# Kernel tuning notes

Measured on AMD Instinct MI355X. Metric: run time of the kernel, lower is better.

The kernel has to match this reference:

```python
import jax, jax.numpy as jnp
import numpy as np

N_DEV, N_CAT, N_APP = 100, 1000, 100000
D = 256
E = 100000

EDGES = [("dev", "app", "ei_dev_app", "ew_dev_app"),
         ("app", "cat", "ei_app_cat", "ew_app_cat"),
         ("app", "app", "ei_app_app", "ew_app_app")]
SIZES = {"dev": N_DEV, "cat": N_CAT, "app": N_APP}


def setup_inputs() -> dict:
    key = jax.random.key(0)
    ks = jax.random.split(key, 32)
    s = 1.0 / np.sqrt(D)
    inp = {
        "x_dev": jax.random.normal(ks[0], (N_DEV, D), jnp.float32),
        "x_cat": jax.random.normal(ks[1], (N_CAT, D), jnp.float32),
        "x_app": jax.random.normal(ks[2], (N_APP, D), jnp.float32),
        "ei_dev_app": jnp.stack([jax.random.randint(ks[3], (E,), 0, N_DEV),
                                 jax.random.randint(ks[4], (E,), 0, N_APP)]).astype(jnp.int32),
        "ei_app_cat": jnp.stack([jax.random.randint(ks[5], (E,), 0, N_APP),
                                 jax.random.randint(ks[6], (E,), 0, N_CAT)]).astype(jnp.int32),
        "ei_app_app": jnp.stack([jax.random.randint(ks[7], (E,), 0, N_APP),
                                 jax.random.randint(ks[8], (E,), 0, N_APP)]).astype(jnp.int32),
        "ew_dev_app": jax.random.uniform(ks[9], (E,), jnp.float32, 0.5, 2.0),
        "ew_app_cat": jax.random.uniform(ks[10], (E,), jnp.float32, 0.5, 2.0),
        "ew_app_app": jax.random.uniform(ks[11], (E,), jnp.float32, 0.5, 2.0),
    }
    # per-node-type linear params for layer1 and layer2 (torch nn.Linear equivalents)
    i = 12
    for layer in (1, 2):
        for t in ("dev", "cat", "app"):
            inp[f"W{layer}_{t}"] = jax.random.normal(ks[i], (D, D), jnp.float32) * s
            inp[f"b{layer}_{t}"] = jax.random.normal(ks[i + 1], (D,), jnp.float32) * s
            i += 2
    return inp


def _mp_layer(x, params, ei, ew):
    """One MyMessagePassing layer: per-src-type linear+relu, edge-weighted
    gather, scatter-add into destination node type."""
    # src-type transform (same math as doing it per edge-type iteration)
    h = {t: jax.nn.relu(x[t] @ params[t][0] + params[t][1]) for t in x}
    out = {t: jnp.zeros((SIZES[t], D), x[t].dtype) for t in x}
    for src, dst, ei_name, ew_name in EDGES:
        idx = ei[ei_name]
        msg = h[src][idx[0]] * ew[ew_name][:, None]  # [E, D]
        out[dst] = out[dst] + jax.ops.segment_sum(msg, idx[1], num_segments=SIZES[dst])
    return out


def reference(x_dev, x_cat, x_app,
              ei_dev_app, ei_app_cat, ei_app_app,
              ew_dev_app, ew_app_cat, ew_app_app,
              W1_dev, b1_dev, W1_cat, b1_cat, W1_app, b1_app,
              W2_dev, b2_dev, W2_cat, b2_cat, W2_app, b2_app):
    ei = {"ei_dev_app": ei_dev_app, "ei_app_cat": ei_app_cat, "ei_app_app": ei_app_app}
    ew = {"ew_dev_app": ew_dev_app, "ew_app_cat": ew_app_cat, "ew_app_app": ew_app_app}
    x = {"dev": x_dev, "cat": x_cat, "app": x_app}
    p1 = {"dev": (W1_dev, b1_dev), "cat": (W1_cat, b1_cat), "app": (W1_app, b1_app)}
    p2 = {"dev": (W2_dev, b2_dev), "cat": (W2_cat, b2_cat), "app": (W2_app, b2_app)}
    x = _mp_layer(x, p1, ei, ew)
    x = _mp_layer(x, p2, ei, ew)
    return (x["dev"], x["cat"], x["app"])
```

## Files before the change

kernel.cpp:

```cpp
#include <hip/hip_runtime.h>
#include <cstdint>
#include <cstddef>

#define DD 256
constexpr int NDEV = 100;
constexpr int NCAT = 1000;
constexpr int NAPP = 100000;
constexpr int NE   = 100000;
constexpr int NCNT = NAPP + NAPP + NCAT;

typedef __attribute__((ext_vector_type(8))) short  bf16x8;
typedef __attribute__((ext_vector_type(8))) unsigned short ushort8;
typedef __attribute__((ext_vector_type(4))) float  f32x4;

__device__ __forceinline__ unsigned short f2bf(float f) {
    unsigned int u = __float_as_uint(f);
    u += 0x7fffu + ((u >> 16) & 1u);
    return (unsigned short)(u >> 16);
}
__device__ __forceinline__ float bf2f(unsigned short h) {
    return __uint_as_float((unsigned int)h << 16);
}

__global__ __launch_bounds__(256)
void wsplit_kernel(const float* __restrict__ W, unsigned short* __restrict__ hi,
                   unsigned short* __restrict__ lo) {
    const int idx = blockIdx.x * 256 + threadIdx.x;
    const int k = idx >> 8, n = idx & 255;
    const float f = W[idx];
    const unsigned short h = f2bf(f);
    hi[n * 256 + k] = h;
    lo[n * 256 + k] = f2bf(f - bf2f(h));
}

#define BK 32
#define PAD 40

__global__ __launch_bounds__(256, 2)
void linear_relu_mfma_kernel(const float* __restrict__ A,
                             const unsigned short* __restrict__ Wt_hi,
                             const unsigned short* __restrict__ Wt_lo,
                             const float* __restrict__ bias,
                             float* __restrict__ C, int M) {
    __shared__ unsigned short As_hi[128][PAD];
    __shared__ unsigned short As_lo[128][PAD];
    __shared__ unsigned short Ws_hi[256][PAD];
    __shared__ unsigned short Ws_lo[256][PAD];

    const int t    = threadIdx.x;
    const int wave = t >> 6;
    const int lane = t & 63;
    const int cl   = lane & 15;
    const int kg8  = (lane >> 4) * 8;
    const int m0   = blockIdx.x * 128;
    const int n0w  = wave * 64;

    f32x4 acc[8][4];
#pragma unroll
    for (int m = 0; m < 8; ++m)
#pragma unroll
        for (int n = 0; n < 4; ++n) acc[m][n] = (f32x4){0.f, 0.f, 0.f, 0.f};

    const int ar = t >> 1;
    const int ak = (t & 1) * 16;

    for (int k0 = 0; k0 < DD; k0 += BK) {
        {
            float fv[16];
            if (m0 + ar < M) {
                const float* p = A + (size_t)(m0 + ar) * DD + k0 + ak;
#pragma unroll
                for (int i = 0; i < 4; ++i) {
                    const float4 v = *(const float4*)(p + i * 4);
                    fv[i * 4 + 0] = v.x; fv[i * 4 + 1] = v.y;
                    fv[i * 4 + 2] = v.z; fv[i * 4 + 3] = v.w;
                }
            } else {
#pragma unroll
                for (int i = 0; i < 16; ++i) fv[i] = 0.f;
            }
#pragma unroll
            for (int g = 0; g < 2; ++g) {
                ushort8 hh, ll;
#pragma unroll
                for (int j = 0; j < 8; ++j) {
                    const float f = fv[g * 8 + j];
                    const unsigned short h = f2bf(f);
                    hh[j] = h;
                    ll[j] = f2bf(f - bf2f(h));
                }
                *(ushort8*)&As_hi[ar][ak + g * 8] = hh;
                *(ushort8*)&As_lo[ar][ak + g * 8] = ll;
            }
        }
        {
            const unsigned short* ph = Wt_hi + (size_t)t * DD + k0;
            const unsigned short* pl = Wt_lo + (size_t)t * DD + k0;
#pragma unroll
            for (int g = 0; g < 4; ++g) {
                *(ushort8*)&Ws_hi[t][g * 8] = *(const ushort8*)(ph + g * 8);
                *(ushort8*)&Ws_lo[t][g * 8] = *(const ushort8*)(pl + g * 8);
            }
        }
        __syncthreads();

        bf16x8 ah[8], al[8], bb[4];
#pragma unroll
        for (int m = 0; m < 8; ++m) {
            ah[m] = *(const bf16x8*)&As_hi[m * 16 + cl][kg8];
            al[m] = *(const bf16x8*)&As_lo[m * 16 + cl][kg8];
        }
#pragma unroll
        for (int n = 0; n < 4; ++n)
            bb[n] = *(const bf16x8*)&Ws_hi[n0w + n * 16 + cl][kg8];
#pragma unroll
        for (int m = 0; m < 8; ++m)
#pragma unroll
            for (int n = 0; n < 4; ++n)
                acc[m][n] = __builtin_amdgcn_mfma_f32_16x16x32_bf16(
                    ah[m], bb[n], acc[m][n], 0, 0, 0);
#pragma unroll
        for (int m = 0; m < 8; ++m)
#pragma unroll
            for (int n = 0; n < 4; ++n)
                acc[m][n] = __builtin_amdgcn_mfma_f32_16x16x32_bf16(
                    al[m], bb[n], acc[m][n], 0, 0, 0);
#pragma unroll
        for (int n = 0; n < 4; ++n)
            bb[n] = *(const bf16x8*)&Ws_lo[n0w + n * 16 + cl][kg8];
#pragma unroll
        for (int m = 0; m < 8; ++m)
#pragma unroll
            for (int n = 0; n < 4; ++n)
                acc[m][n] = __builtin_amdgcn_mfma_f32_16x16x32_bf16(
                    ah[m], bb[n], acc[m][n], 0, 0, 0);
        __syncthreads();
    }

    const int r4 = (lane >> 4) << 2;
#pragma unroll
    for (int n = 0; n < 4; ++n) {
        const int col = n0w + n * 16 + cl;
        const float bv = bias[col];
#pragma unroll
        for (int m = 0; m < 8; ++m) {
            const int rowb = m0 + m * 16 + r4;
            float* cp = C + (size_t)rowb * DD + col;
#pragma unroll
            for (int j = 0; j < 4; ++j)
                if (rowb + j < M) cp[(size_t)j * DD] = fmaxf(acc[m][n][j] + bv, 0.f);
        }
    }
}

__global__ __launch_bounds__(256)
void linear_relu_kernel(const float* __restrict__ A, const float* __restrict__ W,
                        const float* __restrict__ bias, float* __restrict__ C,
                        int M) {
    __shared__ float As[8][128];
    __shared__ float Bs[8][128];

    const int t  = threadIdx.x;
    const int m0 = blockIdx.x * 128;
    const int n0 = blockIdx.y * 128;
    const int ra = (t >> 4) << 2;
    const int ca = (t & 15) << 2;

    float acc[8][8];
#pragma unroll
    for (int i = 0; i < 8; ++i)
#pragma unroll
        for (int j = 0; j < 8; ++j) acc[i][j] = 0.f;

    for (int k0 = 0; k0 < DD; k0 += 8) {
        {
            const int row = t >> 1;
            const int kk  = (t & 1) << 2;
            float4 v = make_float4(0.f, 0.f, 0.f, 0.f);
            if (m0 + row < M)
                v = *(const float4*)(A + (size_t)(m0 + row) * DD + k0 + kk);
            As[kk + 0][row] = v.x;
            As[kk + 1][row] = v.y;
            As[kk + 2][row] = v.z;
            As[kk + 3][row] = v.w;
        }
        {
            const int kk = t >> 5;
            const int nn = (t & 31) << 2;
            *(float4*)&Bs[kk][nn] =
                *(const float4*)(W + (size_t)(k0 + kk) * DD + n0 + nn);
        }
        __syncthreads();
#pragma unroll
        for (int k = 0; k < 8; ++k) {
            const float4 a0 = *(const float4*)&As[k][ra];
            const float4 a1 = *(const float4*)&As[k][ra + 64];
            const float4 b0 = *(const float4*)&Bs[k][ca];
            const float4 b1 = *(const float4*)&Bs[k][ca + 64];
            const float av[8] = {a0.x, a0.y, a0.z, a0.w, a1.x, a1.y, a1.z, a1.w};
            const float bv[8] = {b0.x, b0.y, b0.z, b0.w, b1.x, b1.y, b1.z, b1.w};
#pragma unroll
            for (int i = 0; i < 8; ++i)
#pragma unroll
                for (int j = 0; j < 8; ++j)
                    acc[i][j] = fmaf(av[i], bv[j], acc[i][j]);
        }
        __syncthreads();
    }

    const float4 bias0 = *(const float4*)(bias + n0 + ca);
    const float4 bias1 = *(const float4*)(bias + n0 + ca + 64);
#pragma unroll
    for (int i = 0; i < 8; ++i) {
        const int row = m0 + ((i < 4) ? (ra + i) : (ra + 64 + i - 4));
        if (row >= M) continue;
        float4 o0, o1;
        o0.x = fmaxf(acc[i][0] + bias0.x, 0.f);
        o0.y = fmaxf(acc[i][1] + bias0.y, 0.f);
        o0.z = fmaxf(acc[i][2] + bias0.z, 0.f);
        o0.w = fmaxf(acc[i][3] + bias0.w, 0.f);
        o1.x = fmaxf(acc[i][4] + bias1.x, 0.f);
        o1.y = fmaxf(acc[i][5] + bias1.y, 0.f);
        o1.z = fmaxf(acc[i][6] + bias1.z, 0.f);
        o1.w = fmaxf(acc[i][7] + bias1.w, 0.f);
        *(float4*)(C + (size_t)row * DD + n0 + ca)      = o0;
        *(float4*)(C + (size_t)row * DD + n0 + ca + 64) = o1;
    }
}

__global__ __launch_bounds__(256)
void hist3_kernel(const int* __restrict__ d_aa, const int* __restrict__ d_da,
                  const int* __restrict__ d_ac, int* __restrict__ counts) {
    const int g = blockIdx.x * 256 + threadIdx.x;
    if (g < NE)            atomicAdd(&counts[d_aa[g]], 1);
    else if (g < 2 * NE)   atomicAdd(&counts[NAPP + d_da[g - NE]], 1);
    else if (g < 3 * NE)   atomicAdd(&counts[2 * NAPP + d_ac[g - 2 * NE]], 1);
}

__global__ __launch_bounds__(256)
void scan_partial_kernel(const int* __restrict__ counts, int* __restrict__ bsum,
                         int n) {
    __shared__ int sd[256];
    const int t   = threadIdx.x;
    const int idx = blockIdx.x * 1024 + t * 4;
    int s = 0;
    if (idx + 3 < n) {
        const int4 c = *(const int4*)(counts + idx);
        s = c.x + c.y + c.z + c.w;
    } else {
        for (int j = 0; j < 4; ++j) if (idx + j < n) s += counts[idx + j];
    }
    sd[t] = s;
    __syncthreads();
    for (int off = 128; off > 0; off >>= 1) {
        if (t < off) sd[t] += sd[t + off];
        __syncthreads();
    }
    if (t == 0) bsum[blockIdx.x] = sd[0];
}

__global__ __launch_bounds__(256)
void scan_bsum_kernel(const int* __restrict__ bsum, int* __restrict__ boff, int nb) {
    __shared__ int sd[256];
    const int t = threadIdx.x;
    const int v = (t < nb) ? bsum[t] : 0;
    sd[t] = v;
    __syncthreads();
    for (int off = 1; off < 256; off <<= 1) {
        const int w = (t >= off) ? sd[t - off] : 0;
        __syncthreads();
        sd[t] += w;
        __syncthreads();
    }
    if (t < nb) boff[t] = sd[t] - v;
}

__global__ __launch_bounds__(256)
void scan_apply_kernel(int* __restrict__ counts, const int* __restrict__ boff,
                       int* __restrict__ rs, int n) {
    __shared__ int sd[256];
    const int t   = threadIdx.x;
    const int idx = blockIdx.x * 1024 + t * 4;
    int c[4] = {0, 0, 0, 0};
    if (idx + 3 < n) {
        const int4 v = *(const int4*)(counts + idx);
        c[0] = v.x; c[1] = v.y; c[2] = v.z; c[3] = v.w;
    } else {
        for (int j = 0; j < 4; ++j) if (idx + j < n) c[j] = counts[idx + j];
    }
    const int s = c[0] + c[1] + c[2] + c[3];
    sd[t] = s;
    __syncthreads();
    for (int off = 1; off < 256; off <<= 1) {
        const int w = (t >= off) ? sd[t - off] : 0;
        __syncthreads();
        sd[t] += w;
        __syncthreads();
    }
    int o = boff[blockIdx.x] + sd[t] - s;
#pragma unroll
    for (int j = 0; j < 4; ++j) {
        const int i = idx + j;
        if (i < n) {
            rs[i]     = o;
            counts[i] = o;
            o += c[j];
            if (i == n - 1) rs[n] = o;
        }
    }
}

__global__ __launch_bounds__(256)
void fill3_kernel(const int* __restrict__ ei_aa, const float* __restrict__ ew_aa,
                  const int* __restrict__ ei_da, const float* __restrict__ ew_da,
                  const int* __restrict__ ei_ac, const float* __restrict__ ew_ac,
                  int* __restrict__ cursor, int* __restrict__ srcs,
                  float* __restrict__ wsorted) {
    const int g = blockIdx.x * 256 + threadIdx.x;
    if (g >= 3 * NE) return;
    const int*   ei;
    const float* ew;
    int e, base;
    if (g < NE)            { ei = ei_aa; ew = ew_aa; e = g;          base = 0; }
    else if (g < 2 * NE)   { ei = ei_da; ew = ew_da; e = g - NE;     base = NAPP; }
    else                   { ei = ei_ac; ew = ew_ac; e = g - 2 * NE; base = 2 * NAPP; }
    const int d   = ei[NE + e];
    const int pos = atomicAdd(&cursor[base + d], 1);
    srcs[pos]    = ei[e];
    wsorted[pos] = ew[e];
}

__global__ __launch_bounds__(256)
void gather_l1_app_kernel(const float* __restrict__ hA, const float* __restrict__ hD,
                          const int* __restrict__ rsA, const int* __restrict__ rsD,
                          const int* __restrict__ s, const float* __restrict__ w,
                          float* __restrict__ out, int ndst) {
    const int d    = (int)((blockIdx.x * 256 + threadIdx.x) >> 6);
    const int lane = threadIdx.x & 63;
    if (d >= ndst) return;
    const int o = lane << 2;
    float4 acc = make_float4(0.f, 0.f, 0.f, 0.f);
    for (int p = rsA[d], pe = rsA[d + 1]; p < pe; ++p) {
        const float  ww = w[p];
        const float4 v  = *(const float4*)(hA + (size_t)s[p] * DD + o);
        acc.x = fmaf(ww, v.x, acc.x);
        acc.y = fmaf(ww, v.y, acc.y);
        acc.z = fmaf(ww, v.z, acc.z);
        acc.w = fmaf(ww, v.w, acc.w);
    }
    for (int p = rsD[d], pe = rsD[d + 1]; p < pe; ++p) {
        const float  ww = w[p];
        const float4 v  = *(const float4*)(hD + (size_t)s[p] * DD + o);
        acc.x = fmaf(ww, v.x, acc.x);
        acc.y = fmaf(ww, v.y, acc.y);
        acc.z = fmaf(ww, v.z, acc.z);
        acc.w = fmaf(ww, v.w, acc.w);
    }
    *(float4*)(out + (size_t)d * DD + o) = acc;
}

__global__ __launch_bounds__(256)
void gather_l2_app_kernel(const float* __restrict__ hA,
                          const int* __restrict__ rsA, const int* __restrict__ rsD,
                          const int* __restrict__ s, const float* __restrict__ w,
                          const float* __restrict__ b2dev,
                          float* __restrict__ out, int ndst) {
    const int d    = (int)((blockIdx.x * 256 + threadIdx.x) >> 6);
    const int lane = threadIdx.x & 63;
    if (d >= ndst) return;
    const int o = lane << 2;
    float4 acc = make_float4(0.f, 0.f, 0.f, 0.f);
    for (int p = rsA[d], pe = rsA[d + 1]; p < pe; ++p) {
        const float  ww = w[p];
        const float4 v  = *(const float4*)(hA + (size_t)s[p] * DD + o);
        acc.x = fmaf(ww, v.x, acc.x);
        acc.y = fmaf(ww, v.y, acc.y);
        acc.z = fmaf(ww, v.z, acc.z);
        acc.w = fmaf(ww, v.w, acc.w);
    }
    float wsum = 0.f;
    for (int p = rsD[d], pe = rsD[d + 1]; p < pe; ++p) wsum += w[p];
    const float4 b = *(const float4*)(b2dev + o);
    acc.x = fmaf(wsum, fmaxf(b.x, 0.f), acc.x);
    acc.y = fmaf(wsum, fmaxf(b.y, 0.f), acc.y);
    acc.z = fmaf(wsum, fmaxf(b.z, 0.f), acc.z);
    acc.w = fmaf(wsum, fmaxf(b.w, 0.f), acc.w);
    *(float4*)(out + (size_t)d * DD + o) = acc;
}

__global__ __launch_bounds__(256)
void gather_cat_kernel(const float* __restrict__ hA,
                       const int* __restrict__ rs, const int* __restrict__ s,
                       const float* __restrict__ w,
                       float* __restrict__ out, int ndst) {
    const int d    = (int)((blockIdx.x * 256 + threadIdx.x) >> 6);
    const int lane = threadIdx.x & 63;
    if (d >= ndst) return;
    const int o = lane << 2;
    float4 acc = make_float4(0.f, 0.f, 0.f, 0.f);
    for (int p = rs[d], pe = rs[d + 1]; p < pe; ++p) {
        const float  ww = w[p];
        const float4 v  = *(const float4*)(hA + (size_t)s[p] * DD + o);
        acc.x = fmaf(ww, v.x, acc.x);
        acc.y = fmaf(ww, v.y, acc.y);
        acc.z = fmaf(ww, v.z, acc.z);
        acc.w = fmaf(ww, v.w, acc.w);
    }
    *(float4*)(out + (size_t)d * DD + o) = acc;
}

extern "C" void kernel_launch(void* const* d_in, const int* in_sizes, int n_in,
                              void* d_out, int out_size, void* d_ws, size_t ws_size,
                              hipStream_t stream) {
    const float* x_dev  = (const float*)d_in[0];
    const float* x_app  = (const float*)d_in[2];
    const int*   ei_da  = (const int*)d_in[3];
    const int*   ei_ac  = (const int*)d_in[4];
    const int*   ei_aa  = (const int*)d_in[5];
    const float* ew_da  = (const float*)d_in[6];
    const float* ew_ac  = (const float*)d_in[7];
    const float* ew_aa  = (const float*)d_in[8];
    const float* W1_dev = (const float*)d_in[9];
    const float* b1_dev = (const float*)d_in[10];
    const float* W1_app = (const float*)d_in[13];
    const float* b1_app = (const float*)d_in[14];
    const float* b2_dev = (const float*)d_in[16];
    const float* W2_app = (const float*)d_in[19];
    const float* b2_app = (const float*)d_in[20];

    float* out     = (float*)d_out;
    float* out_cat = out + (size_t)NDEV * DD;
    float* out_app = out + (size_t)(NDEV + NCAT) * DD;

    float* h_app  = (float*)d_ws;
    float* h_dev  = h_app + (size_t)NAPP * DD;
    int*   counts = (int*)(h_dev + (size_t)NDEV * DD);
    int*   rs_all = counts + NCNT;
    int*   s_all  = rs_all + NCNT + 1;
    float* w_all  = (float*)(s_all + 3 * NE);
    int*   bsum   = (int*)(w_all + 3 * NE);
    int*   boff   = bsum + 256;

    int* rs_aa = rs_all;
    int* rs_da = rs_all + NAPP;
    int* rs_ac = rs_all + 2 * NAPP;

    unsigned short* wt1_hi = (unsigned short*)counts;
    unsigned short* wt1_lo = wt1_hi + 65536;
    unsigned short* wt2_hi = wt1_lo + 65536;
    unsigned short* wt2_lo = wt2_hi + 65536;

    const int  nblk = (NCNT + 1023) / 1024;
    const int  gMfma = (NAPP + 127) / 128;
    const int  gGatherApp = (NAPP + 3) / 4;
    const int  gGatherCat = (NCAT + 3) / 4;
    const int  g3e = (3 * NE + 255) / 256;

    hipMemsetAsync(counts, 0, (size_t)NCNT * sizeof(int), stream);
    hist3_kernel<<<g3e, 256, 0, stream>>>(ei_aa + NE, ei_da + NE, ei_ac + NE, counts);
    scan_partial_kernel<<<nblk, 256, 0, stream>>>(counts, bsum, NCNT);
    scan_bsum_kernel<<<1, 256, 0, stream>>>(bsum, boff, nblk);
    scan_apply_kernel<<<nblk, 256, 0, stream>>>(counts, boff, rs_all, NCNT);
    fill3_kernel<<<g3e, 256, 0, stream>>>(ei_aa, ew_aa, ei_da, ew_da, ei_ac, ew_ac,
                                          counts, s_all, w_all);

    wsplit_kernel<<<256, 256, 0, stream>>>(W1_app, wt1_hi, wt1_lo);
    wsplit_kernel<<<256, 256, 0, stream>>>(W2_app, wt2_hi, wt2_lo);

    linear_relu_mfma_kernel<<<gMfma, 256, 0, stream>>>(x_app, wt1_hi, wt1_lo,
                                                       b1_app, h_app, NAPP);
    linear_relu_kernel<<<dim3(1, 2), 256, 0, stream>>>(x_dev, W1_dev, b1_dev,
                                                       h_dev, NDEV);
    gather_l1_app_kernel<<<gGatherApp, 256, 0, stream>>>(
        h_app, h_dev, rs_aa, rs_da, s_all, w_all, out_app, NAPP);

    linear_relu_mfma_kernel<<<gMfma, 256, 0, stream>>>(out_app, wt2_hi, wt2_lo,
                                                       b2_app, h_app, NAPP);
    gather_l2_app_kernel<<<gGatherApp, 256, 0, stream>>>(
        h_app, rs_aa, rs_da, s_all, w_all, b2_dev, out_app, NAPP);
    gather_cat_kernel<<<gGatherCat, 256, 0, stream>>>(
        h_app, rs_ac, s_all, w_all, out_cat, NCAT);

    hipMemsetAsync(out, 0, (size_t)NDEV * DD * sizeof(float), stream);
}
```

Measured before the change: 641.2 us.

## Retile split-bf16 MFMA GEMM to 128x128 blocks with register-prefetched A tiles

The linear+relu MFMA kernel now uses a 2D grid with 128x128 output tiles and a 2x2 wave layout, each wave computing 64x64. Weight fragments are read straight from global memory (L2-resident) instead of being staged in LDS, and the A tile for the next k-step is prefetched into registers while MFMAs run. LDS shrinks to the A hi/lo tiles in an MFMA-friendly layout, so occupancy can rise to 3 blocks per CU. The cost is that A is converted twice (once per column block) and more global weight loads are issued.

```diff
diff --git a/kernel.cpp b/kernel.cpp
--- a/kernel.cpp
+++ b/kernel.cpp
@@ -33,118 +33,129 @@
     lo[n * 256 + k] = f2bf(f - bf2f(h));
 }
 
-#define BK 32
-#define PAD 40
-
-__global__ __launch_bounds__(256, 2)
+__global__ __launch_bounds__(256, 3)
 void linear_relu_mfma_kernel(const float* __restrict__ A,
                              const unsigned short* __restrict__ Wt_hi,
                              const unsigned short* __restrict__ Wt_lo,
                              const float* __restrict__ bias,
                              float* __restrict__ C, int M) {
-    __shared__ unsigned short As_hi[128][PAD];
-    __shared__ unsigned short As_lo[128][PAD];
-    __shared__ unsigned short Ws_hi[256][PAD];
-    __shared__ unsigned short Ws_lo[256][PAD];
+    __shared__ unsigned short As_hi[4096];
+    __shared__ unsigned short As_lo[4096];
 
     const int t    = threadIdx.x;
-    const int wave = t >> 6;
+    const int wid  = t >> 6;
     const int lane = t & 63;
+    const int wr   = wid >> 1;
+    const int wc   = wid & 1;
     const int cl   = lane & 15;
-    const int kg8  = (lane >> 4) * 8;
+    const int kg   = lane >> 4;
     const int m0   = blockIdx.x * 128;
-    const int n0w  = wave * 64;
-
-    f32x4 acc[8][4];
-#pragma unroll
-    for (int m = 0; m < 8; ++m)
+    const int nb   = blockIdx.y * 128 + wc * 64;
+
+    const int loff = kg * 128 + cl * 8;
+
+    const int sr = t >> 1;
+    const int sk = (t & 1) * 16;
+    const bool arow_ok = (m0 + sr) < M;
+    const float* ap = A + (size_t)(m0 + sr) * DD + sk;
+    const int wbase = (sr >> 4) * 512 + (sr & 15) * 8;
+    const int kgw   = (sk >> 3);
+
+    f32x4 acc[4][4];
+#pragma unroll
+    for (int m = 0; m < 4; ++m)
 #pragma unroll
         for (int n = 0; n < 4; ++n) acc[m][n] = (f32x4){0.f, 0.f, 0.f, 0.f};
 
-    const int ar = t >> 1;
-    const int ak = (t & 1) * 16;
-
-    for (int k0 = 0; k0 < DD; k0 += BK) {
-        {
-            float fv[16];
-            if (m0 + ar < M) {
-                const float* p = A + (size_t)(m0 + ar) * DD + k0 + ak;
-#pragma unroll
-                for (int i = 0; i < 4; ++i) {
-                    const float4 v = *(const float4*)(p + i * 4);
-                    fv[i * 4 + 0] = v.x; fv[i * 4 + 1] = v.y;
-                    fv[i * 4 + 2] = v.z; fv[i * 4 + 3] = v.w;
-                }
-            } else {
-#pragma unroll
-                for (int i = 0; i < 16; ++i) fv[i] = 0.f;
-            }
-#pragma unroll
-            for (int g = 0; g < 2; ++g) {
-                ushort8 hh, ll;
-#pragma unroll
-                for (int j = 0; j < 8; ++j) {
-                    const float f = fv[g * 8 + j];
-                    const unsigned short h = f2bf(f);
-                    hh[j] = h;
-                    ll[j] = f2bf(f - bf2f(h));
-                }
-                *(ushort8*)&As_hi[ar][ak + g * 8] = hh;
-                *(ushort8*)&As_lo[ar][ak + g * 8] = ll;
-            }
-        }
-        {
-            const unsigned short* ph = Wt_hi + (size_t)t * DD + k0;
-            const unsigned short* pl = Wt_lo + (size_t)t * DD + k0;
-#pragma unroll
-            for (int g = 0; g < 4; ++g) {
-                *(ushort8*)&Ws_hi[t][g * 8] = *(const ushort8*)(ph + g * 8);
-                *(ushort8*)&Ws_lo[t][g * 8] = *(const ushort8*)(pl + g * 8);
-            }
-        }
-        __syncthreads();
-
-        bf16x8 ah[8], al[8], bb[4];
-#pragma unroll
-        for (int m = 0; m < 8; ++m) {
-            ah[m] = *(const bf16x8*)&As_hi[m * 16 + cl][kg8];
-            al[m] = *(const bf16x8*)&As_lo[m * 16 + cl][kg8];
-        }
-#pragma unroll
-        for (int n = 0; n < 4; ++n)
-            bb[n] = *(const bf16x8*)&Ws_hi[n0w + n * 16 + cl][kg8];
-#pragma unroll
-        for (int m = 0; m < 8; ++m)
+    float pf[16];
+#define LOADT(K0)                                                       \
+    do {                                                                \
+        if (arow_ok) {                                                  \
+            _Pragma("unroll")                                           \
+            for (int i = 0; i < 4; ++i) {                               \
+                const float4 v = *(const float4*)(ap + (K0) + i * 4);   \
+                pf[i * 4 + 0] = v.x; pf[i * 4 + 1] = v.y;               \
+                pf[i * 4 + 2] = v.z; pf[i * 4 + 3] = v.w;               \
+            }                                                           \
+        } else {                                                        \
+            _Pragma("unroll")                                           \
+            for (int i = 0; i < 16; ++i) pf[i] = 0.f;                   \
+        }                                                               \
+    } while (0)
+
+#define WRITET()                                                        \
+    do {                                                                \
+        _Pragma("unroll")                                               \
+        for (int g = 0; g < 2; ++g) {                                   \
+            ushort8 hh, ll;                                             \
+            _Pragma("unroll")                                           \
+            for (int j = 0; j < 8; ++j) {                               \
+                const float f = pf[g * 8 + j];                          \
+                const unsigned short h = f2bf(f);                       \
+                hh[j] = h;                                              \
+                ll[j] = f2bf(f - bf2f(h));                              \
+            }                                                           \
+            *(ushort8*)&As_hi[wbase + (kgw + g) * 128] = hh;            \
+            *(ushort8*)&As_lo[wbase + (kgw + g) * 128] = ll;            \
+        }                                                               \
+    } while (0)
+
+    LOADT(0);
+    WRITET();
+    __syncthreads();
+
+    for (int it = 0; it < 8; ++it) {
+        const int k0 = it * 32;
+        if (it < 7) LOADT(k0 + 32);
+
+        bf16x8 ah[4], al[4], bh[4], bl[4];
+#pragma unroll
+        for (int m = 0; m < 4; ++m) {
+            ah[m] = *(const bf16x8*)&As_hi[(wr * 4 + m) * 512 + loff];
+            al[m] = *(const bf16x8*)&As_lo[(wr * 4 + m) * 512 + loff];
+        }
+#pragma unroll
+        for (int n = 0; n < 4; ++n) {
+            const size_t wo = (size_t)(nb + n * 16 + cl) * DD + k0 + kg * 8;
+            bh[n] = *(const bf16x8*)(Wt_hi + wo);
+            bl[n] = *(const bf16x8*)(Wt_lo + wo);
+        }
+#pragma unroll
+        for (int m = 0; m < 4; ++m)
 #pragma unroll
             for (int n = 0; n < 4; ++n)
                 acc[m][n] = __builtin_amdgcn_mfma_f32_16x16x32_bf16(
-                    ah[m], bb[n], acc[m][n], 0, 0, 0);
-#pragma unroll
-        for (int m = 0; m < 8; ++m)
+                    ah[m], bh[n], acc[m][n], 0, 0, 0);
+#pragma unroll
+        for (int m = 0; m < 4; ++m)
 #pragma unroll
             for (int n = 0; n < 4; ++n)
                 acc[m][n] = __builtin_amdgcn_mfma_f32_16x16x32_bf16(
-                    al[m], bb[n], acc[m][n], 0, 0, 0);
-#pragma unroll
-        for (int n = 0; n < 4; ++n)
-            bb[n] = *(const bf16x8*)&Ws_lo[n0w + n * 16 + cl][kg8];
-#pragma unroll
-        for (int m = 0; m < 8; ++m)
+                    al[m], bh[n], acc[m][n], 0, 0, 0);
+#pragma unroll
+        for (int m = 0; m < 4; ++m)
 #pragma unroll
             for (int n = 0; n < 4; ++n)
                 acc[m][n] = __builtin_amdgcn_mfma_f32_16x16x32_bf16(
-                    ah[m], bb[n], acc[m][n], 0, 0, 0);
-        __syncthreads();
-    }
-
-    const int r4 = (lane >> 4) << 2;
+                    ah[m], bl[n], acc[m][n], 0, 0, 0);
+
+        __syncthreads();
+        if (it < 7) {
+            WRITET();
+            __syncthreads();
+        }
+    }
+#undef LOADT
+#undef WRITET
+
+    const int r4 = kg << 2;
 #pragma unroll
     for (int n = 0; n < 4; ++n) {
-        const int col = n0w + n * 16 + cl;
+        const int col = nb + n * 16 + cl;
         const float bv = bias[col];
 #pragma unroll
-        for (int m = 0; m < 8; ++m) {
-            const int rowb = m0 + m * 16 + r4;
+        for (int m = 0; m < 4; ++m) {
+            const int rowb = m0 + wr * 64 + m * 16 + r4;
             float* cp = C + (size_t)rowb * DD + col;
 #pragma unroll
             for (int j = 0; j < 4; ++j)
@@ -451,7 +462,7 @@
     unsigned short* wt2_lo = wt2_hi + 65536;
 
     const int  nblk = (NCNT + 1023) / 1024;
-    const int  gMfma = (NAPP + 127) / 128;
+    const dim3 gMfma((NAPP + 127) / 128, 2);
     const int  gGatherApp = (NAPP + 3) / 4;
     const int  gGatherCat = (NCAT + 3) / 4;
     const int  g3e = (3 * NE + 255) / 256;
```

Measured after the change: 656.5 us. 2.4% more time.
